# Kernel optimization log

Hardware: AMD Instinct MI355X
Metric: run time of the kernel (lower is better)

Reference implementation:

```python
import jax, jax.numpy as jnp
import numpy as np

N_NODES = 100000
N_EDGES = 1600000
HIDDEN = 100
NUM_CLASSES = 8
NUM_GRAPHS = 128


def setup_inputs() -> dict:
    key = jax.random.key(0)
    ks = jax.random.split(key, 8)
    x = jax.random.normal(ks[0], (N_NODES, 1), dtype=jnp.float32)
    edge_index = jax.random.randint(ks[1], (2, N_EDGES), 0, N_NODES, dtype=jnp.int64)
    batch = jnp.sort(jax.random.randint(ks[2], (N_NODES,), 0, NUM_GRAPHS, dtype=jnp.int64))
    # Glorot-ish init for weights, zero biases (PyG GCNConv default: glorot W, zeros b)
    W1 = jax.random.normal(ks[3], (1, HIDDEN), dtype=jnp.float32) * 0.5
    W2 = jax.random.normal(ks[4], (HIDDEN, HIDDEN), dtype=jnp.float32) * (1.0 / np.sqrt(HIDDEN))
    W3 = jax.random.normal(ks[5], (HIDDEN, HIDDEN), dtype=jnp.float32) * (1.0 / np.sqrt(HIDDEN))
    Wl = jax.random.normal(ks[6], (HIDDEN, NUM_CLASSES), dtype=jnp.float32) * (1.0 / np.sqrt(HIDDEN))
    b1 = jnp.zeros((HIDDEN,), jnp.float32)
    b2 = jnp.zeros((HIDDEN,), jnp.float32)
    b3 = jnp.zeros((HIDDEN,), jnp.float32)
    bl = jnp.zeros((NUM_CLASSES,), jnp.float32)
    return {"x": x, "edge_index": edge_index, "batch": batch,
            "W1": W1, "b1": b1, "W2": W2, "b2": b2, "W3": W3, "b3": b3,
            "Wl": Wl, "bl": bl}


def _gcn_norm(edge_index, n_nodes):
    # Add self-loops, then symmetric normalization D^-1/2 (A+I) D^-1/2
    loop = jnp.arange(n_nodes, dtype=edge_index.dtype)
    src = jnp.concatenate([edge_index[0], loop])
    dst = jnp.concatenate([edge_index[1], loop])
    deg = jax.ops.segment_sum(jnp.ones_like(dst, dtype=jnp.float32), dst,
                              num_segments=n_nodes)
    dinv = jax.lax.rsqrt(deg)  # deg >= 1 thanks to self-loops
    norm = dinv[src] * dinv[dst]  # [E+N]
    return src, dst, norm


def _gcn_conv(x, W, b, src, dst, norm, n_nodes):
    h = x @ W                                   # [N, out]
    msg = h[src] * norm[:, None]                # gather + scale, [E+N, out]
    agg = jax.ops.segment_sum(msg, dst, num_segments=n_nodes)  # scatter-add
    return agg + b


def reference(x, edge_index, batch, W1, b1, W2, b2, W3, b3, Wl, bl):
    n = x.shape[0]
    src, dst, norm = _gcn_norm(edge_index, n)
    h = jax.nn.relu(_gcn_conv(x, W1, b1, src, dst, norm, n))
    h = jax.nn.relu(_gcn_conv(h, W2, b2, src, dst, norm, n))
    h = _gcn_conv(h, W3, b3, src, dst, norm, n)
    # global mean pool over batch segments
    sums = jax.ops.segment_sum(h, batch, num_segments=NUM_GRAPHS)
    counts = jax.ops.segment_sum(jnp.ones((n,), jnp.float32), batch,
                                 num_segments=NUM_GRAPHS)
    pooled = sums / jnp.maximum(counts, 1.0)[:, None]
    return pooled @ Wl + bl  # [NUM_GRAPHS, NUM_CLASSES]
```

## Files before the change

kernel.cpp:

```cpp
#include <hip/hip_runtime.h>

#define N_NODES 100000
#define N_EDGES 1600000
#define HID 100
#define NG 128
#define NC 8
#define NSCAN 391
#define XCD 8
#define SLICE_NODES 12500

static __global__ void init_k(int* __restrict__ degi, float* __restrict__ pooled) {
  int i = blockIdx.x * blockDim.x + threadIdx.x;
  if (i < N_NODES) degi[i] = 1;
  if (i < NG * HID) pooled[i] = 0.0f;
}

static __global__ void deg_k(const int* __restrict__ ei, int* __restrict__ degi) {
  int slice = blockIdx.x & (XCD - 1);
  int lo = slice * SLICE_NODES;
  int hi = min(lo + SLICE_NODES, N_NODES);
  int bid = blockIdx.x >> 3;
  int stride = (gridDim.x >> 3) * blockDim.x;
  for (int e = bid * blockDim.x + threadIdx.x; e < N_EDGES; e += stride) {
    int d = ei[N_EDGES + e];
    if (d >= lo && d < hi) atomicAdd(&degi[d], 1);
  }
}

static __global__ void dinv_k(const int* __restrict__ degi, const float* __restrict__ x,
                              float* __restrict__ dinv, float* __restrict__ xs) {
  int i = blockIdx.x * blockDim.x + threadIdx.x;
  if (i < N_NODES) {
    float d = 1.0f / sqrtf((float)degi[i]);
    dinv[i] = d;
    xs[i] = x[i] * d;
  }
}

static __global__ void reduce_k(const int* __restrict__ degi, int* __restrict__ bsum) {
  int i = blockIdx.x * 256 + threadIdx.x;
  int v = (i < N_NODES) ? degi[i] - 1 : 0;
#pragma unroll
  for (int d = 32; d > 0; d >>= 1) v += __shfl_down(v, d, 64);
  __shared__ int ws[4];
  if ((threadIdx.x & 63) == 0) ws[threadIdx.x >> 6] = v;
  __syncthreads();
  if (threadIdx.x == 0) bsum[blockIdx.x] = ws[0] + ws[1] + ws[2] + ws[3];
}

static __global__ void scanb_k(const int* __restrict__ bsum, int* __restrict__ bpre) {
  __shared__ int s[NSCAN];
  int t = threadIdx.x;
  for (int i = t; i < NSCAN; i += blockDim.x) s[i] = bsum[i];
  __syncthreads();
  if (t == 0) {
    int run = 0;
    for (int i = 0; i < NSCAN; ++i) { int v = s[i]; s[i] = run; run += v; }
  }
  __syncthreads();
  for (int i = t; i < NSCAN; i += blockDim.x) bpre[i] = s[i];
}

static __global__ void rowptr_k(const int* __restrict__ degi, const int* __restrict__ bpre,
                                int* __restrict__ rowptr, int* __restrict__ cursor) {
  int tid = threadIdx.x;
  int i = blockIdx.x * 256 + tid;
  int lane = tid & 63;
  int v = (i < N_NODES) ? degi[i] - 1 : 0;
  int x = v;
#pragma unroll
  for (int d = 1; d < 64; d <<= 1) {
    int t = __shfl_up(x, d, 64);
    if (lane >= d) x += t;
  }
  __shared__ int wsum[4];
  if (lane == 63) wsum[tid >> 6] = x;
  __syncthreads();
  int add = bpre[blockIdx.x];
  for (int w = 0; w < (tid >> 6); ++w) add += wsum[w];
  int incl = x + add;
  if (i < N_NODES) {
    int excl = incl - v;
    rowptr[i] = excl;
    cursor[i] = excl;
  }
  if (i == N_NODES - 1) rowptr[N_NODES] = incl;
}

static __global__ void fill_k(const int* __restrict__ ei, int* __restrict__ cursor,
                              int* __restrict__ col) {
  int slice = blockIdx.x & (XCD - 1);
  int lo = slice * SLICE_NODES;
  int hi = min(lo + SLICE_NODES, N_NODES);
  int bid = blockIdx.x >> 3;
  int stride = (gridDim.x >> 3) * blockDim.x;
  for (int e = bid * blockDim.x + threadIdx.x; e < N_EDGES; e += stride) {
    int s = ei[e];
    int d = ei[N_EDGES + e];
    if (d >= lo && d < hi) {
      int pos = atomicAdd(&cursor[d], 1);
      col[pos] = s;
    }
  }
}

static __global__ void sagg_k(const int* __restrict__ rowptr, const int* __restrict__ col,
                              const float* __restrict__ xs, const float* __restrict__ dinv,
                              float2* __restrict__ pairs) {
  int n = blockIdx.x * blockDim.x + threadIdx.x;
  if (n >= N_NODES) return;
  float s = xs[n];
  int e0 = rowptr[n], e1 = rowptr[n + 1];
  int e = e0;
  for (; e + 4 <= e1; e += 4) {
    float v0 = xs[col[e]], v1 = xs[col[e + 1]], v2 = xs[col[e + 2]], v3 = xs[col[e + 3]];
    s += v0 + v1 + v2 + v3;
  }
  for (; e < e1; ++e) s += xs[col[e]];
  float di = dinv[n];
  pairs[n] = make_float2(s * di, di);
}

static __global__ __launch_bounds__(256) void l12_k(
    const int* __restrict__ rowptr, const int* __restrict__ col,
    const float2* __restrict__ pairs, const float* __restrict__ W1,
    const float* __restrict__ b1, float4* __restrict__ G4) {
  int node = blockIdx.x * 8 + (threadIdx.x >> 5);
  int q = threadIdx.x & 31;
  if (node >= N_NODES || q >= 25) return;
  float4 w = reinterpret_cast<const float4*>(W1)[q];
  float4 b = reinterpret_cast<const float4*>(b1)[q];
  float2 self = pairs[node];
  float4 acc;
  acc.x = self.y * fmaxf(fmaf(self.x, w.x, b.x), 0.0f);
  acc.y = self.y * fmaxf(fmaf(self.x, w.y, b.y), 0.0f);
  acc.z = self.y * fmaxf(fmaf(self.x, w.z, b.z), 0.0f);
  acc.w = self.y * fmaxf(fmaf(self.x, w.w, b.w), 0.0f);
  int e0 = rowptr[node], e1 = rowptr[node + 1];
  int e = e0;
#pragma unroll 1
  for (; e + 4 <= e1; e += 4) {
    float2 p0 = pairs[col[e]];
    float2 p1 = pairs[col[e + 1]];
    float2 p2 = pairs[col[e + 2]];
    float2 p3 = pairs[col[e + 3]];
    acc.x = fmaf(p0.y, fmaxf(fmaf(p0.x, w.x, b.x), 0.0f), acc.x);
    acc.y = fmaf(p0.y, fmaxf(fmaf(p0.x, w.y, b.y), 0.0f), acc.y);
    acc.z = fmaf(p0.y, fmaxf(fmaf(p0.x, w.z, b.z), 0.0f), acc.z);
    acc.w = fmaf(p0.y, fmaxf(fmaf(p0.x, w.w, b.w), 0.0f), acc.w);
    acc.x = fmaf(p1.y, fmaxf(fmaf(p1.x, w.x, b.x), 0.0f), acc.x);
    acc.y = fmaf(p1.y, fmaxf(fmaf(p1.x, w.y, b.y), 0.0f), acc.y);
    acc.z = fmaf(p1.y, fmaxf(fmaf(p1.x, w.z, b.z), 0.0f), acc.z);
    acc.w = fmaf(p1.y, fmaxf(fmaf(p1.x, w.w, b.w), 0.0f), acc.w);
    acc.x = fmaf(p2.y, fmaxf(fmaf(p2.x, w.x, b.x), 0.0f), acc.x);
    acc.y = fmaf(p2.y, fmaxf(fmaf(p2.x, w.y, b.y), 0.0f), acc.y);
    acc.z = fmaf(p2.y, fmaxf(fmaf(p2.x, w.z, b.z), 0.0f), acc.z);
    acc.w = fmaf(p2.y, fmaxf(fmaf(p2.x, w.w, b.w), 0.0f), acc.w);
    acc.x = fmaf(p3.y, fmaxf(fmaf(p3.x, w.x, b.x), 0.0f), acc.x);
    acc.y = fmaf(p3.y, fmaxf(fmaf(p3.x, w.y, b.y), 0.0f), acc.y);
    acc.z = fmaf(p3.y, fmaxf(fmaf(p3.x, w.z, b.z), 0.0f), acc.z);
    acc.w = fmaf(p3.y, fmaxf(fmaf(p3.x, w.w, b.w), 0.0f), acc.w);
  }
  for (; e < e1; ++e) {
    float2 p = pairs[col[e]];
    acc.x = fmaf(p.y, fmaxf(fmaf(p.x, w.x, b.x), 0.0f), acc.x);
    acc.y = fmaf(p.y, fmaxf(fmaf(p.x, w.y, b.y), 0.0f), acc.y);
    acc.z = fmaf(p.y, fmaxf(fmaf(p.x, w.z, b.z), 0.0f), acc.z);
    acc.w = fmaf(p.y, fmaxf(fmaf(p.x, w.w, b.w), 0.0f), acc.w);
  }
  float di = self.y;
  G4[node * 25 + q] = make_float4(acc.x * di, acc.y * di, acc.z * di, acc.w * di);
}

static __global__ __launch_bounds__(256) void agg4_k(
    const int* __restrict__ rowptr, const int* __restrict__ col,
    const float4* __restrict__ B4, const float* __restrict__ dinv,
    float4* __restrict__ out4) {
  int node = blockIdx.x * 8 + (threadIdx.x >> 5);
  int q = threadIdx.x & 31;
  if (node >= N_NODES || q >= 25) return;
  float4 acc = B4[node * 25 + q];
  int e0 = rowptr[node], e1 = rowptr[node + 1];
  int e = e0;
#pragma unroll 1
  for (; e + 4 <= e1; e += 4) {
    int s0 = col[e], s1 = col[e + 1], s2 = col[e + 2], s3 = col[e + 3];
    float4 v0 = B4[s0 * 25 + q];
    float4 v1 = B4[s1 * 25 + q];
    float4 v2 = B4[s2 * 25 + q];
    float4 v3 = B4[s3 * 25 + q];
    acc.x += v0.x + v1.x + v2.x + v3.x;
    acc.y += v0.y + v1.y + v2.y + v3.y;
    acc.z += v0.z + v1.z + v2.z + v3.z;
    acc.w += v0.w + v1.w + v2.w + v3.w;
  }
  for (; e < e1; ++e) {
    float4 v = B4[col[e] * 25 + q];
    acc.x += v.x; acc.y += v.y; acc.z += v.z; acc.w += v.w;
  }
  float di = dinv[node];
  out4[node * 25 + q] = make_float4(acc.x * di, acc.y * di, acc.z * di, acc.w * di);
}

static __global__ __launch_bounds__(256) void gemm2_k(
    const float* __restrict__ G, const float* __restrict__ W,
    const float* __restrict__ bias, const float* __restrict__ dinv,
    float* __restrict__ Bout) {
  __shared__ float tile[64 * 101];
  const int nb = blockIdx.x * 64;
#pragma unroll
  for (int i = 0; i < 25; ++i) {
    int flat = i * 256 + threadIdx.x;
    int n = flat / 100, j = flat - n * 100;
    float v = 0.0f;
    if (nb + n < N_NODES) v = G[(size_t)(nb + n) * 100 + j];
    tile[n * 101 + j] = v;
  }
  __syncthreads();
  const int lane = threadIdx.x & 63;
  const int kc = __builtin_amdgcn_readfirstlane(threadIdx.x >> 6);
  const int n = nb + lane;
  float acc[25];
#pragma unroll
  for (int k = 0; k < 25; ++k) acc[k] = 0.0f;
  const float* trow = &tile[lane * 101];
  const float* wbase = W + kc * 25;
#pragma unroll 4
  for (int j = 0; j < 100; ++j) {
    float wv[25];
    const float* wr = wbase + j * 100;
#pragma unroll
    for (int k = 0; k < 25; ++k) wv[k] = wr[k];
    const float hj = trow[j];
#pragma unroll
    for (int k = 0; k < 25; ++k) acc[k] = fmaf(hj, wv[k], acc[k]);
  }
  if (n < N_NODES) {
    const float di = dinv[n];
    const int base = n * 100 + kc * 25;
#pragma unroll
    for (int k = 0; k < 25; ++k) {
      float v = fmaxf(acc[k] + bias[kc * 25 + k], 0.0f) * di;
      Bout[base + k] = v;
    }
  }
}

static __device__ int lb(const int* __restrict__ a, int n, int v) {
  int lo = 0, hi = n;
  while (lo < hi) { int m = (lo + hi) >> 1; if (a[m] < v) lo = m + 1; else hi = m; }
  return lo;
}

#define PSLICES 8
static __global__ void pool2_k(const float* __restrict__ A, const int* __restrict__ batch,
                               float* __restrict__ pooled, float* __restrict__ counts) {
  int g = blockIdx.x;
  int slice = blockIdx.y;
  int k = threadIdx.x;
  int lo = lb(batch, N_NODES, g);
  int hi = lb(batch, N_NODES, g + 1);
  int cnt = hi - lo;
  if (slice == 0 && k == 0) counts[g] = (float)cnt;
  int per = (cnt + PSLICES - 1) / PSLICES;
  int s0 = lo + slice * per;
  int s1 = min(s0 + per, hi);
  if (k < HID && s1 > s0) {
    float s = 0.0f;
    for (int n = s0; n < s1; ++n) s += A[n * HID + k];
    atomicAdd(&pooled[g * HID + k], s);
  }
}

static __global__ void head2_k(const float* __restrict__ pooled, const float* __restrict__ counts,
                               const float* __restrict__ W3, const float* __restrict__ b3,
                               const float* __restrict__ Wl, const float* __restrict__ bl,
                               float* __restrict__ out) {
  __shared__ float t1[HID];
  int g = blockIdx.x;
  int t = threadIdx.x;
  float inv = 1.0f / fmaxf(counts[g], 1.0f);
  if (t < HID) {
    float acc = 0.0f;
#pragma unroll 4
    for (int j = 0; j < HID; ++j)
      acc = fmaf(pooled[g * HID + j] * inv, W3[j * HID + t], acc);
    t1[t] = acc + b3[t];
  }
  __syncthreads();
  if (t < NC) {
    float acc = 0.0f;
#pragma unroll 4
    for (int j = 0; j < HID; ++j)
      acc = fmaf(t1[j], Wl[j * NC + t], acc);
    out[g * NC + t] = acc + bl[t];
  }
}

extern "C" void kernel_launch(void* const* d_in, const int* in_sizes, int n_in,
                              void* d_out, int out_size, void* d_ws, size_t ws_size,
                              hipStream_t stream) {
  const float* x    = (const float*)d_in[0];
  const int* ei     = (const int*)d_in[1];
  const int* batch  = (const int*)d_in[2];
  const float* W1   = (const float*)d_in[3];
  const float* b1   = (const float*)d_in[4];
  const float* W2   = (const float*)d_in[5];
  const float* b2   = (const float*)d_in[6];
  const float* W3   = (const float*)d_in[7];
  const float* b3   = (const float*)d_in[8];
  const float* Wl   = (const float*)d_in[9];
  const float* bl   = (const float*)d_in[10];
  float* out = (float*)d_out;

  char* p = (char*)d_ws;
  auto alloc = [&](size_t bytes) {
    char* q = p;
    p += (bytes + 255) & ~(size_t)255;
    return q;
  };
  float* dinv   = (float*)alloc((size_t)N_NODES * 4);
  float* xs     = (float*)alloc((size_t)N_NODES * 4);
  float2* pairs = (float2*)alloc((size_t)N_NODES * 8);
  int*   degi   = (int*)alloc((size_t)N_NODES * 4);
  int*   rowptr = (int*)alloc((size_t)(N_NODES + 1) * 4);
  int*   cursor = (int*)alloc((size_t)N_NODES * 4);
  int*   bsum   = (int*)alloc((size_t)NSCAN * 4);
  int*   bpre   = (int*)alloc((size_t)NSCAN * 4);
  int*   col    = (int*)alloc((size_t)N_EDGES * 4);
  float* B      = (float*)alloc((size_t)N_NODES * HID * 4);
  float* G      = (float*)alloc((size_t)N_NODES * HID * 4);
  float* pooled = (float*)alloc((size_t)NG * HID * 4);
  float* counts = (float*)alloc((size_t)NG * 4);

  const int T = 256;
  int gN   = (N_NODES + T - 1) / T;
  int gAgg = (N_NODES + 7) / 8;
  int gGemm = (N_NODES + 63) / 64;

  init_k<<<gN, T, 0, stream>>>(degi, pooled);
  deg_k<<<2048, T, 0, stream>>>(ei, degi);
  dinv_k<<<gN, T, 0, stream>>>(degi, x, dinv, xs);
  reduce_k<<<NSCAN, 256, 0, stream>>>(degi, bsum);
  scanb_k<<<1, 256, 0, stream>>>(bsum, bpre);
  rowptr_k<<<NSCAN, 256, 0, stream>>>(degi, bpre, rowptr, cursor);
  fill_k<<<2048, T, 0, stream>>>(ei, cursor, col);

  sagg_k<<<gN, T, 0, stream>>>(rowptr, col, xs, dinv, pairs);

  l12_k<<<gAgg, T, 0, stream>>>(rowptr, col, pairs, W1, b1, (float4*)G);
  gemm2_k<<<gGemm, T, 0, stream>>>(G, W2, b2, dinv, B);

  agg4_k<<<gAgg, T, 0, stream>>>(rowptr, col, (const float4*)B, dinv, (float4*)G);

  pool2_k<<<dim3(NG, PSLICES), 128, 0, stream>>>(G, batch, pooled, counts);
  head2_k<<<NG, 128, 0, stream>>>(pooled, counts, W3, b3, Wl, bl, out);
}
```

Measured before the change: 442.4 us.

## Replace final-layer aggregation and pooling with source-side push into per-block graph sums

The third layer's gather-aggregate over a 100-wide feature matrix, followed by mean pooling, is replaced by a source-ordered CSR whose edges carry each destination's graph id and degree scale. Each source node's features are pushed into per-block shared-memory pooled sums with LDS atomics, and the per-block partials are then reduced. This avoids writing and re-reading the full N x 100 aggregated matrix and the separate pool pass. In exchange it builds a second CSR (extra atomics and an 8-byte-per-edge array), relies on heavy shared-memory atomic contention, and adds a reduction over 512 partial copies. The GEMM output layout is also interleaved to match the new read pattern.

```diff
diff --git a/kernel.cpp b/kernel.cpp
--- a/kernel.cpp
+++ b/kernel.cpp
@@ -8,22 +8,20 @@
 #define NSCAN 391
 #define XCD 8
 #define SLICE_NODES 12500
-
-static __global__ void init_k(int* __restrict__ degi, float* __restrict__ pooled) {
-  int i = blockIdx.x * blockDim.x + threadIdx.x;
-  if (i < N_NODES) degi[i] = 1;
-  if (i < NG * HID) pooled[i] = 0.0f;
-}
-
-static __global__ void deg_k(const int* __restrict__ ei, int* __restrict__ degi) {
+#define PUSH_BLOCKS 512
+
+static __global__ void degb_k(const int* __restrict__ ei, int* __restrict__ degi,
+                              int* __restrict__ degs) {
   int slice = blockIdx.x & (XCD - 1);
   int lo = slice * SLICE_NODES;
   int hi = min(lo + SLICE_NODES, N_NODES);
   int bid = blockIdx.x >> 3;
   int stride = (gridDim.x >> 3) * blockDim.x;
   for (int e = bid * blockDim.x + threadIdx.x; e < N_EDGES; e += stride) {
+    int s = ei[e];
     int d = ei[N_EDGES + e];
     if (d >= lo && d < hi) atomicAdd(&degi[d], 1);
+    if (s >= lo && s < hi) atomicAdd(&degs[s], 1);
   }
 }
 
@@ -31,42 +29,50 @@
                               float* __restrict__ dinv, float* __restrict__ xs) {
   int i = blockIdx.x * blockDim.x + threadIdx.x;
   if (i < N_NODES) {
-    float d = 1.0f / sqrtf((float)degi[i]);
+    float d = 1.0f / sqrtf(1.0f + (float)degi[i]);
     dinv[i] = d;
     xs[i] = x[i] * d;
   }
 }
 
-static __global__ void reduce_k(const int* __restrict__ degi, int* __restrict__ bsum) {
+static __global__ void reduce_k(const int* __restrict__ degi, const int* __restrict__ degs,
+                                int* __restrict__ bsum) {
+  const int* a = blockIdx.y ? degs : degi;
   int i = blockIdx.x * 256 + threadIdx.x;
-  int v = (i < N_NODES) ? degi[i] - 1 : 0;
+  int v = (i < N_NODES) ? a[i] : 0;
 #pragma unroll
   for (int d = 32; d > 0; d >>= 1) v += __shfl_down(v, d, 64);
   __shared__ int ws[4];
   if ((threadIdx.x & 63) == 0) ws[threadIdx.x >> 6] = v;
   __syncthreads();
-  if (threadIdx.x == 0) bsum[blockIdx.x] = ws[0] + ws[1] + ws[2] + ws[3];
+  if (threadIdx.x == 0) bsum[blockIdx.y * NSCAN + blockIdx.x] = ws[0] + ws[1] + ws[2] + ws[3];
 }
 
 static __global__ void scanb_k(const int* __restrict__ bsum, int* __restrict__ bpre) {
   __shared__ int s[NSCAN];
+  int base = blockIdx.x * NSCAN;
   int t = threadIdx.x;
-  for (int i = t; i < NSCAN; i += blockDim.x) s[i] = bsum[i];
+  for (int i = t; i < NSCAN; i += blockDim.x) s[i] = bsum[base + i];
   __syncthreads();
   if (t == 0) {
     int run = 0;
     for (int i = 0; i < NSCAN; ++i) { int v = s[i]; s[i] = run; run += v; }
   }
   __syncthreads();
-  for (int i = t; i < NSCAN; i += blockDim.x) bpre[i] = s[i];
-}
-
-static __global__ void rowptr_k(const int* __restrict__ degi, const int* __restrict__ bpre,
-                                int* __restrict__ rowptr, int* __restrict__ cursor) {
+  for (int i = t; i < NSCAN; i += blockDim.x) bpre[base + i] = s[i];
+}
+
+static __global__ void rowptr_k(const int* __restrict__ degi, const int* __restrict__ degs,
+                                const int* __restrict__ bpre,
+                                int* __restrict__ rowptr, int* __restrict__ cursor,
+                                int* __restrict__ rowptr2, int* __restrict__ cursor2) {
+  const int* a = blockIdx.y ? degs : degi;
+  int* rp = blockIdx.y ? rowptr2 : rowptr;
+  int* cu = blockIdx.y ? cursor2 : cursor;
   int tid = threadIdx.x;
   int i = blockIdx.x * 256 + tid;
   int lane = tid & 63;
-  int v = (i < N_NODES) ? degi[i] - 1 : 0;
+  int v = (i < N_NODES) ? a[i] : 0;
   int x = v;
 #pragma unroll
   for (int d = 1; d < 64; d <<= 1) {
@@ -76,19 +82,21 @@
   __shared__ int wsum[4];
   if (lane == 63) wsum[tid >> 6] = x;
   __syncthreads();
-  int add = bpre[blockIdx.x];
+  int add = bpre[blockIdx.y * NSCAN + blockIdx.x];
   for (int w = 0; w < (tid >> 6); ++w) add += wsum[w];
   int incl = x + add;
   if (i < N_NODES) {
     int excl = incl - v;
-    rowptr[i] = excl;
-    cursor[i] = excl;
-  }
-  if (i == N_NODES - 1) rowptr[N_NODES] = incl;
-}
-
-static __global__ void fill_k(const int* __restrict__ ei, int* __restrict__ cursor,
-                              int* __restrict__ col) {
+    rp[i] = excl;
+    cu[i] = excl;
+  }
+  if (i == N_NODES - 1) rp[N_NODES] = incl;
+}
+
+static __global__ void fillb_k(const int* __restrict__ ei, const int* __restrict__ batch,
+                               const float* __restrict__ dinv,
+                               int* __restrict__ cursor, int* __restrict__ col,
+                               int* __restrict__ cursor2, int2* __restrict__ col2) {
   int slice = blockIdx.x & (XCD - 1);
   int lo = slice * SLICE_NODES;
   int hi = min(lo + SLICE_NODES, N_NODES);
@@ -100,6 +108,10 @@
     if (d >= lo && d < hi) {
       int pos = atomicAdd(&cursor[d], 1);
       col[pos] = s;
+    }
+    if (s >= lo && s < hi) {
+      int pos = atomicAdd(&cursor2[s], 1);
+      col2[pos] = make_int2(batch[d], __float_as_int(dinv[d]));
     }
   }
 }
@@ -172,36 +184,6 @@
   G4[node * 25 + q] = make_float4(acc.x * di, acc.y * di, acc.z * di, acc.w * di);
 }
 
-static __global__ __launch_bounds__(256) void agg4_k(
-    const int* __restrict__ rowptr, const int* __restrict__ col,
-    const float4* __restrict__ B4, const float* __restrict__ dinv,
-    float4* __restrict__ out4) {
-  int node = blockIdx.x * 8 + (threadIdx.x >> 5);
-  int q = threadIdx.x & 31;
-  if (node >= N_NODES || q >= 25) return;
-  float4 acc = B4[node * 25 + q];
-  int e0 = rowptr[node], e1 = rowptr[node + 1];
-  int e = e0;
-#pragma unroll 1
-  for (; e + 4 <= e1; e += 4) {
-    int s0 = col[e], s1 = col[e + 1], s2 = col[e + 2], s3 = col[e + 3];
-    float4 v0 = B4[s0 * 25 + q];
-    float4 v1 = B4[s1 * 25 + q];
-    float4 v2 = B4[s2 * 25 + q];
-    float4 v3 = B4[s3 * 25 + q];
-    acc.x += v0.x + v1.x + v2.x + v3.x;
-    acc.y += v0.y + v1.y + v2.y + v3.y;
-    acc.z += v0.z + v1.z + v2.z + v3.z;
-    acc.w += v0.w + v1.w + v2.w + v3.w;
-  }
-  for (; e < e1; ++e) {
-    float4 v = B4[col[e] * 25 + q];
-    acc.x += v.x; acc.y += v.y; acc.z += v.z; acc.w += v.w;
-  }
-  float di = dinv[node];
-  out4[node * 25 + q] = make_float4(acc.x * di, acc.y * di, acc.z * di, acc.w * di);
-}
-
 static __global__ __launch_bounds__(256) void gemm2_k(
     const float* __restrict__ G, const float* __restrict__ W,
     const float* __restrict__ bias, const float* __restrict__ dinv,
@@ -237,13 +219,61 @@
   }
   if (n < N_NODES) {
     const float di = dinv[n];
-    const int base = n * 100 + kc * 25;
+    const int base = n * 100;
 #pragma unroll
     for (int k = 0; k < 25; ++k) {
       float v = fmaxf(acc[k] + bias[kc * 25 + k], 0.0f) * di;
-      Bout[base + k] = v;
+      Bout[base + 4 * k + kc] = v;
     }
   }
+}
+
+static __global__ __launch_bounds__(256) void push_k(
+    const int* __restrict__ rowptr2, const int2* __restrict__ col2,
+    const float4* __restrict__ B4, const int* __restrict__ batch,
+    const float* __restrict__ dinv, float* __restrict__ partials) {
+  __shared__ float pl[NG * HID];
+  for (int i = threadIdx.x; i < NG * HID; i += 256) pl[i] = 0.0f;
+  __syncthreads();
+  int grp = threadIdx.x >> 5;
+  int q = threadIdx.x & 31;
+  if (q < 25) {
+    for (int oct = blockIdx.x; oct * 8 < N_NODES; oct += PUSH_BLOCKS) {
+      int node = oct * 8 + grp;
+      if (node >= N_NODES) continue;
+      float4 r = B4[node * 25 + q];
+      {
+        float c = dinv[node];
+        float* base = &pl[batch[node] * HID];
+        atomicAdd(&base[q],      c * r.x);
+        atomicAdd(&base[q + 25], c * r.y);
+        atomicAdd(&base[q + 50], c * r.z);
+        atomicAdd(&base[q + 75], c * r.w);
+      }
+      int e0 = rowptr2[node], e1 = rowptr2[node + 1];
+      for (int e = e0; e < e1; ++e) {
+        int2 tc = col2[e];
+        float c = __int_as_float(tc.y);
+        float* base = &pl[tc.x * HID];
+        atomicAdd(&base[q],      c * r.x);
+        atomicAdd(&base[q + 25], c * r.y);
+        atomicAdd(&base[q + 50], c * r.z);
+        atomicAdd(&base[q + 75], c * r.w);
+      }
+    }
+  }
+  __syncthreads();
+  float* dst = partials + (size_t)blockIdx.x * (NG * HID);
+  for (int i = threadIdx.x; i < NG * HID; i += 256) dst[i] = pl[i];
+}
+
+static __global__ void redpart_k(const float* __restrict__ partials,
+                                 float* __restrict__ pooled) {
+  int i = blockIdx.x * blockDim.x + threadIdx.x;
+  if (i >= NG * HID) return;
+  float s = 0.0f;
+  for (int b = 0; b < PUSH_BLOCKS; ++b) s += partials[(size_t)b * (NG * HID) + i];
+  pooled[i] = s;
 }
 
 static __device__ int lb(const int* __restrict__ a, int n, int v) {
@@ -252,34 +282,16 @@
   return lo;
 }
 
-#define PSLICES 8
-static __global__ void pool2_k(const float* __restrict__ A, const int* __restrict__ batch,
-                               float* __restrict__ pooled, float* __restrict__ counts) {
-  int g = blockIdx.x;
-  int slice = blockIdx.y;
-  int k = threadIdx.x;
-  int lo = lb(batch, N_NODES, g);
-  int hi = lb(batch, N_NODES, g + 1);
-  int cnt = hi - lo;
-  if (slice == 0 && k == 0) counts[g] = (float)cnt;
-  int per = (cnt + PSLICES - 1) / PSLICES;
-  int s0 = lo + slice * per;
-  int s1 = min(s0 + per, hi);
-  if (k < HID && s1 > s0) {
-    float s = 0.0f;
-    for (int n = s0; n < s1; ++n) s += A[n * HID + k];
-    atomicAdd(&pooled[g * HID + k], s);
-  }
-}
-
-static __global__ void head2_k(const float* __restrict__ pooled, const float* __restrict__ counts,
+static __global__ void head2_k(const float* __restrict__ pooled, const int* __restrict__ batch,
                                const float* __restrict__ W3, const float* __restrict__ b3,
                                const float* __restrict__ Wl, const float* __restrict__ bl,
                                float* __restrict__ out) {
   __shared__ float t1[HID];
   int g = blockIdx.x;
   int t = threadIdx.x;
-  float inv = 1.0f / fmaxf(counts[g], 1.0f);
+  int lo = lb(batch, N_NODES, g);
+  int hi = lb(batch, N_NODES, g + 1);
+  float inv = 1.0f / fmaxf((float)(hi - lo), 1.0f);
   if (t < HID) {
     float acc = 0.0f;
 #pragma unroll 4
@@ -319,40 +331,46 @@
     p += (bytes + 255) & ~(size_t)255;
     return q;
   };
-  float* dinv   = (float*)alloc((size_t)N_NODES * 4);
-  float* xs     = (float*)alloc((size_t)N_NODES * 4);
-  float2* pairs = (float2*)alloc((size_t)N_NODES * 8);
-  int*   degi   = (int*)alloc((size_t)N_NODES * 4);
-  int*   rowptr = (int*)alloc((size_t)(N_NODES + 1) * 4);
-  int*   cursor = (int*)alloc((size_t)N_NODES * 4);
-  int*   bsum   = (int*)alloc((size_t)NSCAN * 4);
-  int*   bpre   = (int*)alloc((size_t)NSCAN * 4);
-  int*   col    = (int*)alloc((size_t)N_EDGES * 4);
-  float* B      = (float*)alloc((size_t)N_NODES * HID * 4);
-  float* G      = (float*)alloc((size_t)N_NODES * HID * 4);
-  float* pooled = (float*)alloc((size_t)NG * HID * 4);
-  float* counts = (float*)alloc((size_t)NG * 4);
+  int*   degi    = (int*)alloc((size_t)N_NODES * 2 * 4);
+  int*   degs    = degi + N_NODES;
+  float* dinv    = (float*)alloc((size_t)N_NODES * 4);
+  float* xs      = (float*)alloc((size_t)N_NODES * 4);
+  float2* pairs  = (float2*)alloc((size_t)N_NODES * 8);
+  int*   rowptr  = (int*)alloc((size_t)(N_NODES + 1) * 4);
+  int*   rowptr2 = (int*)alloc((size_t)(N_NODES + 1) * 4);
+  int*   cursor  = (int*)alloc((size_t)N_NODES * 4);
+  int*   cursor2 = (int*)alloc((size_t)N_NODES * 4);
+  int*   bsum    = (int*)alloc((size_t)NSCAN * 2 * 4);
+  int*   bpre    = (int*)alloc((size_t)NSCAN * 2 * 4);
+  int*   col     = (int*)alloc((size_t)N_EDGES * 4);
+  int2*  col2    = (int2*)alloc((size_t)N_EDGES * 8);
+  float* B       = (float*)alloc((size_t)N_NODES * HID * 4);
+  float* G       = (float*)alloc((size_t)N_NODES * HID * 4);
+  float* partials= (float*)alloc((size_t)PUSH_BLOCKS * NG * HID * 4);
+  float* pooled  = (float*)alloc((size_t)NG * HID * 4);
 
   const int T = 256;
   int gN   = (N_NODES + T - 1) / T;
   int gAgg = (N_NODES + 7) / 8;
   int gGemm = (N_NODES + 63) / 64;
 
-  init_k<<<gN, T, 0, stream>>>(degi, pooled);
-  deg_k<<<2048, T, 0, stream>>>(ei, degi);
+  (void)hipMemsetAsync(degi, 0, (size_t)N_NODES * 2 * 4, stream);
+  degb_k<<<2048, T, 0, stream>>>(ei, degi, degs);
   dinv_k<<<gN, T, 0, stream>>>(degi, x, dinv, xs);
-  reduce_k<<<NSCAN, 256, 0, stream>>>(degi, bsum);
-  scanb_k<<<1, 256, 0, stream>>>(bsum, bpre);
-  rowptr_k<<<NSCAN, 256, 0, stream>>>(degi, bpre, rowptr, cursor);
-  fill_k<<<2048, T, 0, stream>>>(ei, cursor, col);
+  reduce_k<<<dim3(NSCAN, 2), 256, 0, stream>>>(degi, degs, bsum);
+  scanb_k<<<2, 256, 0, stream>>>(bsum, bpre);
+  rowptr_k<<<dim3(NSCAN, 2), 256, 0, stream>>>(degi, degs, bpre, rowptr, cursor,
+                                               rowptr2, cursor2);
+  fillb_k<<<2048, T, 0, stream>>>(ei, batch, dinv, cursor, col, cursor2, col2);
 
   sagg_k<<<gN, T, 0, stream>>>(rowptr, col, xs, dinv, pairs);
 
   l12_k<<<gAgg, T, 0, stream>>>(rowptr, col, pairs, W1, b1, (float4*)G);
   gemm2_k<<<gGemm, T, 0, stream>>>(G, W2, b2, dinv, B);
 
-  agg4_k<<<gAgg, T, 0, stream>>>(rowptr, col, (const float4*)B, dinv, (float4*)G);
-
-  pool2_k<<<dim3(NG, PSLICES), 128, 0, stream>>>(G, batch, pooled, counts);
-  head2_k<<<NG, 128, 0, stream>>>(pooled, counts, W3, b3, Wl, bl, out);
-}
+  push_k<<<PUSH_BLOCKS, T, 0, stream>>>(rowptr2, col2, (const float4*)B, batch,
+                                        dinv, partials);
+  redpart_k<<<(NG * HID + T - 1) / T, T, 0, stream>>>(partials, pooled);
+
+  head2_k<<<NG, 128, 0, stream>>>(pooled, batch, W3, b3, Wl, bl, out);
+}
```

Result: slower. 1.331 ms (+200.8%).
